# Optimization experiments

Measured on AMD Instinct MI355X. Metric: run time of the kernel, lower is better.

Reference implementation:

```python
import jax, jax.numpy as jnp
import numpy as np

EPS = 1e-5
N_HEADS = 8


def _ln(x, g, b):
    m = jnp.mean(x, -1, keepdims=True)
    v = jnp.mean((x - m) ** 2, -1, keepdims=True)
    return (x - m) * jax.lax.rsqrt(v + EPS) * g + b


def setup_inputs() -> dict:
    key = jax.random.key(0)
    ks = jax.random.split(key, 24)
    B, T, H = 64, 512, 256
    HH, H2 = H // 2, 2 * H
    w = lambda k, shape, fan_in: jax.random.normal(k, shape, jnp.float32) / np.sqrt(fan_in)
    return {
        "state": jax.random.normal(ks[0], (B, T, H), jnp.float32),
        "action": jax.random.normal(ks[1], (B, T, 2), jnp.float32),
        "ae_w1": w(ks[2], (2, HH), 2), "ae_b1": jnp.zeros((HH,), jnp.float32),
        "ae_w2": w(ks[3], (HH, H), HH), "ae_b2": jnp.zeros((H,), jnp.float32),
        "ln1_g": jnp.ones((H,), jnp.float32), "ln1_b": jnp.zeros((H,), jnp.float32),
        "ln2_g": jnp.ones((H,), jnp.float32), "ln2_b": jnp.zeros((H,), jnp.float32),
        "wq": w(ks[4], (H, H), H), "bq": jnp.zeros((H,), jnp.float32),
        "wk": w(ks[5], (H, H), H), "bk": jnp.zeros((H,), jnp.float32),
        "wv": w(ks[6], (H, H), H), "bv": jnp.zeros((H,), jnp.float32),
        "wo": w(ks[7], (H, H), H), "bo": jnp.zeros((H,), jnp.float32),
        "gru_wih": w(ks[8], (H, 3 * H2), H), "gru_bih": jnp.zeros((3 * H2,), jnp.float32),
        "gru_whh": w(ks[9], (H2, 3 * H2), H2), "gru_bhh": jnp.zeros((3 * H2,), jnp.float32),
        "mlp_w": w(ks[10], (H2, H), H2), "mlp_b": jnp.zeros((H,), jnp.float32),
    }


def reference(state, action, ae_w1, ae_b1, ae_w2, ae_b2, ln1_g, ln1_b, ln2_g, ln2_b,
              wq, bq, wk, bk, wv, bv, wo, bo,
              gru_wih, gru_bih, gru_whh, gru_bhh, mlp_w, mlp_b):
    B, T, H = state.shape
    dH = H // N_HEADS
    # action encoder (vectorized over all timesteps at once)
    ae = jax.nn.relu(action @ ae_w1 + ae_b1) @ ae_w2 + ae_b2  # [B,T,H]
    q_in = _ln(state, ln1_g, ln1_b)
    kv_in = _ln(ae, ln2_g, ln2_b)
    qh = (q_in @ wq + bq).reshape(B, T, N_HEADS, dH)
    kh = (kv_in @ wk + bk).reshape(B, T, N_HEADS, dH)
    vh = (kv_in @ wv + bv).reshape(B, T, N_HEADS, dH)
    # single query / single key per (b,t): softmax over the length-1 key axis == 1
    scores = jnp.sum(qh * kh, -1, keepdims=True) / jnp.sqrt(jnp.asarray(dH, state.dtype))
    attn = jax.nn.softmax(scores, axis=-1)  # [B,T,nH,1] of ones
    attended = (attn * vh).reshape(B, T, H) @ wo + bo
    x = state + attended  # [B,T,H]
    # GRU: original uses batch_first=False on a [B,T,H] tensor, so the
    # recurrence runs over dim 0 (B) with T as the effective batch.
    H2 = gru_whh.shape[0]

    def step(h, x_t):  # h,[T,2H]; x_t [T,H]
        gi = x_t @ gru_wih + gru_bih
        gh = h @ gru_whh + gru_bhh
        i_r, i_z, i_n = jnp.split(gi, 3, -1)
        h_r, h_z, h_n = jnp.split(gh, 3, -1)
        r = jax.nn.sigmoid(i_r + h_r)
        z = jax.nn.sigmoid(i_z + h_z)
        n = jnp.tanh(i_n + r * h_n)
        h_new = (1.0 - z) * n + z * h
        return h_new, h_new

    h0 = jnp.zeros((T, H2), x.dtype)
    _, out = jax.lax.scan(step, h0, x)  # [B,T,2H]
    states = out @ mlp_w + mlp_b  # dropout is identity in eval mode
    return states, states[:, -1]
```

## Files before the change

kernel.cpp:

```cpp
#include <hip/hip_runtime.h>
#include <hip/hip_bf16.h>

typedef unsigned short u16;
typedef unsigned long long u64;
typedef __attribute__((ext_vector_type(8))) short bf16x8;
typedef __attribute__((ext_vector_type(4))) float f32x4;

static __device__ __forceinline__ u16 f2bf(float f) {
    union { float f; unsigned u; } cv; cv.f = f;
    unsigned u = cv.u;
    unsigned r = u + 0x7FFF + ((u >> 16) & 1);
    return (u16)(r >> 16);
}
static __device__ __forceinline__ float bf2f(u16 b) {
    union { unsigned u; float f; } cv; cv.u = ((unsigned)b) << 16;
    return cv.f;
}
static __device__ __forceinline__ float sigmoidf_(float x) {
    return 1.0f / (1.0f + __expf(-x));
}
static __device__ __forceinline__ float tanhf_(float x) {
    float e = __expf(-2.f * fabsf(x));
    float t = (1.f - e) / (1.f + e);
    return copysignf(t, x);
}

__global__ __launch_bounds__(256) void prep_all(
    const float* __restrict__ wv, const float* __restrict__ wo,
    const float* __restrict__ wih, const float* __restrict__ whh,
    const float* __restrict__ mlp, const float* __restrict__ w2,
    const float* __restrict__ bv, const float* __restrict__ bo,
    u16* __restrict__ WfT, u16* __restrict__ wihT,
    u16* __restrict__ whhT, u16* __restrict__ mlpT, u16* __restrict__ w2T,
    float* __restrict__ bfv, u16* __restrict__ h0_bf,
    unsigned* __restrict__ flags)
{
    __shared__ u16 t[64][66];
    int bid = blockIdx.x, tid = threadIdx.x;

    if (bid >= 458) {
        int j = bid - 458, i = tid;
        float s = 0.f;
        for (int k = 0; k < 256; ++k) s = fmaf(wv[i * 256 + k], wo[k * 256 + j], s);
        WfT[j * 256 + i] = f2bf(s);
        return;
    }
    if (bid == 328) {
        int j = tid;
        float s = bo[j];
        for (int k = 0; k < 256; ++k) s = fmaf(bv[k], wo[k * 256 + j], s);
        bfv[j] = s;
        return;
    }
    if (bid >= 329 && bid < 457) {
        int i = ((bid - 329) * 256 + tid) * 2;
        u64* p = (u64*)h0_bf;
        p[i] = 0; p[i + 1] = 0;
        return;
    }
    if (bid == 457) {
        unsigned* p = flags;
        for (int i = tid; i < 32 * 8 * 32; i += 256) p[i] = 0u;
        return;
    }

    const float* src; u16* dst; int K, N, bx, by;
    if (bid < 96)       { src = wih; dst = wihT; K = 256; N = 1536; int l = bid;       bx = l & 3; by = l >> 2; }
    else if (bid < 288) { src = whh; dst = whhT; K = 512; N = 1536; int l = bid - 96;  bx = l & 7; by = l >> 3; }
    else if (bid < 320) { src = mlp; dst = mlpT; K = 512; N = 256;  int l = bid - 288; bx = l & 7; by = l >> 3; }
    else                { src = w2;  dst = w2T;  K = 128; N = 256;  int l = bid - 320; bx = l & 1; by = l >> 1; }

    int k0 = bx * 64, n0 = by * 64;
    int r = tid >> 4, c4 = (tid & 15) * 4;
#pragma unroll
    for (int p = 0; p < 4; ++p) {
        int row = r + p * 16;
        float4 v = *(const float4*)&src[(size_t)(k0 + row) * N + n0 + c4];
        t[c4 + 0][row] = f2bf(v.x);
        t[c4 + 1][row] = f2bf(v.y);
        t[c4 + 2][row] = f2bf(v.z);
        t[c4 + 3][row] = f2bf(v.w);
    }
    __syncthreads();
    int rr = tid >> 3, cc = (tid & 7) * 8;
#pragma unroll
    for (int p = 0; p < 2; ++p) {
        int row = rr + p * 32;
        u16 pack[8];
#pragma unroll
        for (int j = 0; j < 8; ++j) pack[j] = t[row][cc + j];
        *(uint4*)&dst[(size_t)(n0 + row) * K + k0 + cc] = *(uint4*)pack;
    }
}

__global__ __launch_bounds__(256) void ae_ln_mfma(
    const float* __restrict__ action,
    const float* __restrict__ w1, const float* __restrict__ b1,
    const u16* __restrict__ w2T, const float* __restrict__ b2,
    const float* __restrict__ g, const float* __restrict__ be,
    u16* __restrict__ kvbf)
{
    __shared__ u16 lB[256][136];
    __shared__ u16 lA[64][136];
    int tid = threadIdx.x;
    long base = (long)blockIdx.x * 64;

    for (int idx = tid; idx < 256 * 16; idx += 256) {
        int r = idx >> 4, ch = (idx & 15) * 8;
        *(uint4*)&lB[r][ch] = *(const uint4*)&w2T[r * 128 + ch];
    }
    for (int idx = tid; idx < 8192; idx += 256) {
        int r = idx >> 7, k = idx & 127;
        float a0 = action[(base + r) * 2], a1 = action[(base + r) * 2 + 1];
        float v = fmaf(a1, w1[128 + k], fmaf(a0, w1[k], b1[k]));
        lA[r][k] = f2bf(v > 0.f ? v : 0.f);
    }
    __syncthreads();

    int wv = tid >> 6, l = tid & 63;
    int fr = l & 15, fq = l >> 4;
    f32x4 acc[4][4] = {};
#pragma unroll
    for (int ks = 0; ks < 4; ++ks) {
        bf16x8 a[4], b[4];
#pragma unroll
        for (int mi = 0; mi < 4; ++mi) a[mi] = *(bf16x8*)&lA[mi * 16 + fr][ks * 32 + fq * 8];
#pragma unroll
        for (int ni = 0; ni < 4; ++ni) b[ni] = *(bf16x8*)&lB[wv * 64 + ni * 16 + fr][ks * 32 + fq * 8];
#pragma unroll
        for (int mi = 0; mi < 4; ++mi)
#pragma unroll
            for (int ni = 0; ni < 4; ++ni)
                acc[mi][ni] = __builtin_amdgcn_mfma_f32_16x16x32_bf16(a[mi], b[ni], acc[mi][ni], 0, 0, 0);
    }
    __syncthreads();

    float* e = (float*)&lB[0][0];
#pragma unroll
    for (int mi = 0; mi < 4; ++mi)
#pragma unroll
        for (int ni = 0; ni < 4; ++ni) {
            int col = wv * 64 + ni * 16 + fr;
            float bb = b2[col];
#pragma unroll
            for (int reg = 0; reg < 4; ++reg)
                e[(mi * 16 + fq * 4 + reg) * 261 + col] = acc[mi][ni][reg] + bb;
        }
    __syncthreads();

    int t = tid >> 2, sub = tid & 3;
    float s = 0.f, ss = 0.f;
#pragma unroll
    for (int i = 0; i < 64; ++i) {
        float v = e[t * 261 + sub + i * 4];
        s += v; ss += v * v;
    }
    s += __shfl_xor(s, 1); ss += __shfl_xor(ss, 1);
    s += __shfl_xor(s, 2); ss += __shfl_xor(ss, 2);
    float m = s * (1.f / 256.f);
    float var = ss * (1.f / 256.f) - m * m;
    float rs = rsqrtf(var + 1e-5f);
#pragma unroll
    for (int i8 = 0; i8 < 8; ++i8) {
        u16 pack[8];
#pragma unroll
        for (int j = 0; j < 8; ++j) {
            int col = sub * 64 + i8 * 8 + j;
            float v = (e[t * 261 + col] - m) * rs * g[col] + be[col];
            pack[j] = f2bf(v);
        }
        *(uint4*)&kvbf[(base + t) * 256 + sub * 64 + i8 * 8] = *(uint4*)pack;
    }
}

template <int MODE>
__global__ __launch_bounds__(256) void gemm128(
    const u16* __restrict__ A, const u16* __restrict__ BT,
    const float* __restrict__ bias, const float* __restrict__ resid,
    u16* __restrict__ outBf, float* __restrict__ outF,
    int N, int K)
{
    __shared__ u16 lA[128][72];
    __shared__ u16 lB[128][72];
    int tid = threadIdx.x;
    int bm = blockIdx.x * 128, bn = blockIdx.y * 128;

    f32x4 acc[4][4] = {};
    int w = tid >> 6, l = tid & 63;
    int wr = (w >> 1) * 64, wc = (w & 1) * 64;
    int fr = l & 15, fk = (l >> 4) * 8;

    for (int k0 = 0; k0 < K; k0 += 64) {
#pragma unroll
        for (int i = 0; i < 4; ++i) {
            int idx = tid + i * 256;
            int r = idx >> 3, c8 = (idx & 7) * 8;
            *(uint4*)&lA[r][c8] = *(const uint4*)&A[(long)(bm + r) * K + k0 + c8];
            *(uint4*)&lB[r][c8] = *(const uint4*)&BT[(long)(bn + r) * K + k0 + c8];
        }
        __syncthreads();
#pragma unroll
        for (int half = 0; half < 2; ++half) {
            int fo = half * 32 + fk;
            bf16x8 a[4], b[4];
#pragma unroll
            for (int mi = 0; mi < 4; ++mi) a[mi] = *(bf16x8*)&lA[wr + mi * 16 + fr][fo];
#pragma unroll
            for (int ni = 0; ni < 4; ++ni) b[ni] = *(bf16x8*)&lB[wc + ni * 16 + fr][fo];
#pragma unroll
            for (int mi = 0; mi < 4; ++mi)
#pragma unroll
                for (int ni = 0; ni < 4; ++ni)
                    acc[mi][ni] = __builtin_amdgcn_mfma_f32_16x16x32_bf16(a[mi], b[ni], acc[mi][ni], 0, 0, 0);
        }
        __syncthreads();
    }

#pragma unroll
    for (int mi = 0; mi < 4; ++mi)
#pragma unroll
        for (int ni = 0; ni < 4; ++ni) {
            int c = bn + wc + ni * 16 + fr;
            float bz = bias[c];
#pragma unroll
            for (int reg = 0; reg < 4; ++reg) {
                int r = bm + wr + mi * 16 + (l >> 4) * 4 + reg;
                float v = acc[mi][ni][reg] + bz;
                if constexpr (MODE == 0) {
                    v += resid[(long)r * N + c];
                    outBf[(long)r * N + c] = f2bf(v);
                } else if constexpr (MODE == 1) {
                    outBf[(long)r * N + c] = f2bf(v);
                } else {
                    outF[(long)r * N + c] = v;
                    if ((r & 511) == 511) outF[8388608 + (long)(r >> 9) * N + c] = v;
                }
            }
        }
}

__global__ __launch_bounds__(768, 1) void gru_persistent6(
    const u16* __restrict__ whhT, const float* __restrict__ bhh,
    const u16* __restrict__ gi_bf, const u16* __restrict__ h0_bf,
    u16* __restrict__ out_bf, unsigned* __restrict__ flags)
{
    __shared__ u64 lh64[2048];
    __shared__ __align__(16) float ghs[3][16][68];
    u16* lh = (u16*)lh64;

    int tid = threadIdx.x;
    int bid = blockIdx.x;
    int tg = bid >> 3, cb = bid & 7;
    int tbase = tg * 16, cbase = cb * 64;

    int w = tid >> 6, l = tid & 63;
    int fr = l & 15, fo = l >> 4;
    int cpos = w & 3, gate = w >> 2;

    bf16x8 a[16];
    {
        const u16* wp = whhT + ((size_t)(gate << 9) + cbase + cpos * 16 + fr) * 512 + fo * 8;
#pragma unroll
        for (int kk = 0; kk < 16; ++kk)
            a[kk] = *(const bf16x8*)(wp + kk * 32);
    }

    int et = tid >> 5, ec = (tid & 31) * 2;
    bool ep = tid < 512;
    float hreg0 = 0.f, hreg1 = 0.f;
    float bh_r0 = 0, bh_r1 = 0, bh_z0 = 0, bh_z1 = 0, bh_n0 = 0, bh_n1 = 0;
    if (ep) {
        bh_r0 = bhh[cbase + ec];        bh_r1 = bhh[cbase + ec + 1];
        bh_z0 = bhh[512 + cbase + ec];  bh_z1 = bhh[512 + cbase + ec + 1];
        bh_n0 = bhh[1024 + cbase + ec]; bh_n1 = bhh[1024 + cbase + ec + 1];
    }

    const unsigned* gp = (const unsigned*)gi_bf;
    unsigned g_r = 0, g_z = 0, g_n = 0;
    if (ep) {
        size_t grow = (size_t)(tbase + et) * 1536;
        g_r = gp[(grow + cbase + ec) >> 1];
        g_z = gp[(grow + 512 + cbase + ec) >> 1];
        g_n = gp[(grow + 1024 + cbase + ec) >> 1];
    }

    for (int step = 0; step < 64; ++step) {
        const u64* hb64 = (const u64*)(step ? out_bf + (size_t)(step - 1) * 262144
                                           : h0_bf);
#pragma unroll
        for (int i = 0; i < 3; ++i) {
            int idx = tid + i * 768;
            if (idx < 2048) {
                int r = idx >> 7, kw = idx & 127;
                u64 v = __hip_atomic_load(hb64 + (size_t)(tbase + r) * 128 + kw,
                                          __ATOMIC_RELAXED, __HIP_MEMORY_SCOPE_AGENT);
                lh64[r * 128 + (kw ^ ((r & 7) << 1))] = v;
            }
        }
        __syncthreads();

        f32x4 acc = {0.f, 0.f, 0.f, 0.f};
#pragma unroll
        for (int kk = 0; kk < 16; ++kk) {
            int kb = kk * 32 + fo * 8;
            bf16x8 b = *(bf16x8*)&lh[fr * 512 + (kb ^ ((fr & 7) << 3))];
            acc = __builtin_amdgcn_mfma_f32_16x16x32_bf16(a[kk], b, acc, 0, 0, 0);
        }
        *(f32x4*)&ghs[gate][fr][cpos * 16 + fo * 4] = acc;
        __syncthreads();

        if (ep) {
            float ghr0 = ghs[0][et][ec], ghr1 = ghs[0][et][ec + 1];
            float ghz0 = ghs[1][et][ec], ghz1 = ghs[1][et][ec + 1];
            float ghn0 = ghs[2][et][ec], ghn1 = ghs[2][et][ec + 1];
            float r0 = sigmoidf_(bf2f((u16)(g_r & 0xffff)) + ghr0 + bh_r0);
            float r1 = sigmoidf_(bf2f((u16)(g_r >> 16)) + ghr1 + bh_r1);
            float z0 = sigmoidf_(bf2f((u16)(g_z & 0xffff)) + ghz0 + bh_z0);
            float z1 = sigmoidf_(bf2f((u16)(g_z >> 16)) + ghz1 + bh_z1);
            float n0 = tanhf_(bf2f((u16)(g_n & 0xffff)) + r0 * (ghn0 + bh_n0));
            float n1 = tanhf_(bf2f((u16)(g_n >> 16)) + r1 * (ghn1 + bh_n1));
            hreg0 = (1.f - z0) * n0 + z0 * hreg0;
            hreg1 = (1.f - z1) * n1 + z1 * hreg1;
            unsigned packv = (unsigned)f2bf(hreg0) | ((unsigned)f2bf(hreg1) << 16);
            __hip_atomic_store(
                (unsigned*)out_bf + ((((size_t)step * 512 + tbase + et) * 512 + cbase + ec) >> 1),
                packv, __ATOMIC_RELAXED, __HIP_MEMORY_SCOPE_AGENT);
        }
        __syncthreads();

        if (step < 63) {
            if (tid == 0)
                __hip_atomic_store(&flags[(tg * 8 + cb) * 32], (unsigned)(step + 1),
                                   __ATOMIC_RELAXED, __HIP_MEMORY_SCOPE_AGENT);
            if (ep) {
                size_t grow = ((size_t)(step + 1) * 512 + tbase + et) * 1536;
                g_r = gp[(grow + cbase + ec) >> 1];
                g_z = gp[(grow + 512 + cbase + ec) >> 1];
                g_n = gp[(grow + 1024 + cbase + ec) >> 1];
            }
            if (tid < 8) {
                unsigned tgt = (unsigned)(step + 1);
                while (__hip_atomic_load(&flags[(tg * 8 + tid) * 32],
                                         __ATOMIC_RELAXED, __HIP_MEMORY_SCOPE_AGENT) < tgt)
                    __builtin_amdgcn_s_sleep(1);
            }
            __syncthreads();
        }
    }
}

extern "C" void kernel_launch(void* const* d_in, const int* in_sizes, int n_in,
                              void* d_out, int out_size, void* d_ws, size_t ws_size,
                              hipStream_t stream)
{
    const float* state   = (const float*)d_in[0];
    const float* action  = (const float*)d_in[1];
    const float* ae_w1   = (const float*)d_in[2];
    const float* ae_b1   = (const float*)d_in[3];
    const float* ae_w2   = (const float*)d_in[4];
    const float* ae_b2   = (const float*)d_in[5];
    const float* ln2_g   = (const float*)d_in[8];
    const float* ln2_b   = (const float*)d_in[9];
    const float* wv      = (const float*)d_in[14];
    const float* bv      = (const float*)d_in[15];
    const float* wo      = (const float*)d_in[16];
    const float* bo      = (const float*)d_in[17];
    const float* gru_wih = (const float*)d_in[18];
    const float* gru_bih = (const float*)d_in[19];
    const float* gru_whh = (const float*)d_in[20];
    const float* gru_bhh = (const float*)d_in[21];
    const float* mlp_w   = (const float*)d_in[22];
    const float* mlp_b   = (const float*)d_in[23];

    char* ws = (char*)d_ws;
    size_t off = 0;
    auto carve = [&](size_t bytes) -> char* {
        char* p = ws + off; off = (off + bytes + 255) & ~(size_t)255; return p;
    };
    u16*   kv_bf  = (u16*)carve(32768ull * 256 * 2);
    u16*   x_bf   = (u16*)carve(32768ull * 256 * 2);
    u16*   gi_bf  = (u16*)carve(32768ull * 1536 * 2);
    u16*   out_bf = (u16*)carve(32768ull * 512 * 2);
    u16*   WfT    = (u16*)carve(256 * 256 * 2);
    float* bfv    = (float*)carve(256 * 4);
    u16*   wihT   = (u16*)carve(1536 * 256 * 2);
    u16*   whhT   = (u16*)carve(1536 * 512 * 2);
    u16*   mlpT   = (u16*)carve(256 * 512 * 2);
    u16*   w2T    = (u16*)carve(256 * 128 * 2);
    u16*   h0_bf  = (u16*)carve(512 * 512 * 2);
    unsigned* flags = (unsigned*)carve(32 * 8 * 32 * 4);

    prep_all<<<714, 256, 0, stream>>>(wv, wo, gru_wih, gru_whh, mlp_w, ae_w2,
                                      bv, bo, WfT, wihT, whhT, mlpT, w2T,
                                      bfv, h0_bf, flags);

    ae_ln_mfma<<<512, 256, 0, stream>>>(action, ae_w1, ae_b1, w2T, ae_b2,
                                        ln2_g, ln2_b, kv_bf);

    gemm128<0><<<dim3(256, 2), 256, 0, stream>>>(kv_bf, WfT, bfv, state, x_bf, nullptr, 256, 256);
    gemm128<1><<<dim3(256, 12), 256, 0, stream>>>(x_bf, wihT, gru_bih, nullptr, gi_bf, nullptr, 1536, 256);

    {
        void* args[] = { (void*)&whhT, (void*)&gru_bhh, (void*)&gi_bf,
                         (void*)&h0_bf, (void*)&out_bf, (void*)&flags };
        hipError_t cerr = hipLaunchCooperativeKernel((const void*)gru_persistent6,
                                                     dim3(256), dim3(768), args, 0, stream);
        if (cerr != hipSuccess) {
            gru_persistent6<<<dim3(256), dim3(768), 0, stream>>>(
                whhT, gru_bhh, gi_bf, h0_bf, out_bf, flags);
        }
    }

    gemm128<2><<<dim3(256, 2), 256, 0, stream>>>(out_bf, mlpT, mlp_b, nullptr, nullptr,
                                                 (float*)d_out, 256, 512);
}
```

Before: 358.4 us.

## Fuse GRU input projection into persistent recurrent kernel

Measured after the change: 606.4 us. 69.2% more time.

```diff
diff --git a/kernel.cpp b/kernel.cpp
--- a/kernel.cpp
+++ b/kernel.cpp
@@ -239,13 +239,15 @@
         }
 }
 
-__global__ __launch_bounds__(768, 1) void gru_persistent6(
-    const u16* __restrict__ whhT, const float* __restrict__ bhh,
-    const u16* __restrict__ gi_bf, const u16* __restrict__ h0_bf,
+__global__ __launch_bounds__(768, 1) void gru_persistent11(
+    const u16* __restrict__ whhT, const u16* __restrict__ wihT,
+    const float* __restrict__ bhh, const float* __restrict__ bih,
+    const u16* __restrict__ x_bf, const u16* __restrict__ h0_bf,
     u16* __restrict__ out_bf, unsigned* __restrict__ flags)
 {
     __shared__ u64 lh64[2048];
     __shared__ __align__(16) float ghs[3][16][68];
+    __shared__ __align__(16) float gis[3][16][68];
     u16* lh = (u16*)lh64;
 
     int tid = threadIdx.x;
@@ -264,25 +266,42 @@
         for (int kk = 0; kk < 16; ++kk)
             a[kk] = *(const bf16x8*)(wp + kk * 32);
     }
+    const u16* wp2 = wihT + ((size_t)(gate << 9) + cbase + cpos * 16 + fr) * 256 + fo * 8;
 
     int et = tid >> 5, ec = (tid & 31) * 2;
     bool ep = tid < 512;
     float hreg0 = 0.f, hreg1 = 0.f;
-    float bh_r0 = 0, bh_r1 = 0, bh_z0 = 0, bh_z1 = 0, bh_n0 = 0, bh_n1 = 0;
+    float bs_r0 = 0, bs_r1 = 0, bs_z0 = 0, bs_z1 = 0;
+    float bi_n0 = 0, bi_n1 = 0, bh_n0 = 0, bh_n1 = 0;
     if (ep) {
-        bh_r0 = bhh[cbase + ec];        bh_r1 = bhh[cbase + ec + 1];
-        bh_z0 = bhh[512 + cbase + ec];  bh_z1 = bhh[512 + cbase + ec + 1];
-        bh_n0 = bhh[1024 + cbase + ec]; bh_n1 = bhh[1024 + cbase + ec + 1];
-    }
-
-    const unsigned* gp = (const unsigned*)gi_bf;
-    unsigned g_r = 0, g_z = 0, g_n = 0;
-    if (ep) {
-        size_t grow = (size_t)(tbase + et) * 1536;
-        g_r = gp[(grow + cbase + ec) >> 1];
-        g_z = gp[(grow + 512 + cbase + ec) >> 1];
-        g_n = gp[(grow + 1024 + cbase + ec) >> 1];
-    }
+        bs_r0 = bih[cbase + ec] + bhh[cbase + ec];
+        bs_r1 = bih[cbase + ec + 1] + bhh[cbase + ec + 1];
+        bs_z0 = bih[512 + cbase + ec] + bhh[512 + cbase + ec];
+        bs_z1 = bih[512 + cbase + ec + 1] + bhh[512 + cbase + ec + 1];
+        bi_n0 = bih[1024 + cbase + ec];  bi_n1 = bih[1024 + cbase + ec + 1];
+        bh_n0 = bhh[1024 + cbase + ec];  bh_n1 = bhh[1024 + cbase + ec + 1];
+    }
+
+    auto gi_compute = [&](int t) {
+        const u16* xp = x_bf + ((size_t)t * 512 + tbase + fr) * 256 + fo * 8;
+        f32x4 gacc = {0.f, 0.f, 0.f, 0.f};
+#pragma unroll
+        for (int half = 0; half < 2; ++half) {
+            bf16x8 xf[4], wf[4];
+#pragma unroll
+            for (int j = 0; j < 4; ++j) {
+                int kk = half * 4 + j;
+                xf[j] = *(const bf16x8*)(xp + kk * 32);
+                wf[j] = *(const bf16x8*)(wp2 + kk * 32);
+            }
+#pragma unroll
+            for (int j = 0; j < 4; ++j)
+                gacc = __builtin_amdgcn_mfma_f32_16x16x32_bf16(wf[j], xf[j], gacc, 0, 0, 0);
+        }
+        *(f32x4*)&gis[gate][fr][cpos * 16 + fo * 4] = gacc;
+    };
+
+    gi_compute(0);
 
     for (int step = 0; step < 64; ++step) {
         const u64* hb64 = (const u64*)(step ? out_bf + (size_t)(step - 1) * 262144
@@ -310,15 +329,12 @@
         __syncthreads();
 
         if (ep) {
-            float ghr0 = ghs[0][et][ec], ghr1 = ghs[0][et][ec + 1];
-            float ghz0 = ghs[1][et][ec], ghz1 = ghs[1][et][ec + 1];
-            float ghn0 = ghs[2][et][ec], ghn1 = ghs[2][et][ec + 1];
-            float r0 = sigmoidf_(bf2f((u16)(g_r & 0xffff)) + ghr0 + bh_r0);
-            float r1 = sigmoidf_(bf2f((u16)(g_r >> 16)) + ghr1 + bh_r1);
-            float z0 = sigmoidf_(bf2f((u16)(g_z & 0xffff)) + ghz0 + bh_z0);
-            float z1 = sigmoidf_(bf2f((u16)(g_z >> 16)) + ghz1 + bh_z1);
-            float n0 = tanhf_(bf2f((u16)(g_n & 0xffff)) + r0 * (ghn0 + bh_n0));
-            float n1 = tanhf_(bf2f((u16)(g_n >> 16)) + r1 * (ghn1 + bh_n1));
+            float r0 = sigmoidf_(gis[0][et][ec]     + ghs[0][et][ec]     + bs_r0);
+            float r1 = sigmoidf_(gis[0][et][ec + 1] + ghs[0][et][ec + 1] + bs_r1);
+            float z0 = sigmoidf_(gis[1][et][ec]     + ghs[1][et][ec]     + bs_z0);
+            float z1 = sigmoidf_(gis[1][et][ec + 1] + ghs[1][et][ec + 1] + bs_z1);
+            float n0 = tanhf_(gis[2][et][ec]     + bi_n0 + r0 * (ghs[2][et][ec]     + bh_n0));
+            float n1 = tanhf_(gis[2][et][ec + 1] + bi_n1 + r1 * (ghs[2][et][ec + 1] + bh_n1));
             hreg0 = (1.f - z0) * n0 + z0 * hreg0;
             hreg1 = (1.f - z1) * n1 + z1 * hreg1;
             unsigned packv = (unsigned)f2bf(hreg0) | ((unsigned)f2bf(hreg1) << 16);
@@ -332,12 +348,7 @@
             if (tid == 0)
                 __hip_atomic_store(&flags[(tg * 8 + cb) * 32], (unsigned)(step + 1),
                                    __ATOMIC_RELAXED, __HIP_MEMORY_SCOPE_AGENT);
-            if (ep) {
-                size_t grow = ((size_t)(step + 1) * 512 + tbase + et) * 1536;
-                g_r = gp[(grow + cbase + ec) >> 1];
-                g_z = gp[(grow + 512 + cbase + ec) >> 1];
-                g_n = gp[(grow + 1024 + cbase + ec) >> 1];
-            }
+            gi_compute(step + 1);
             if (tid < 8) {
                 unsigned tgt = (unsigned)(step + 1);
                 while (__hip_atomic_load(&flags[(tg * 8 + tid) * 32],
@@ -379,7 +390,6 @@
     };
     u16*   kv_bf  = (u16*)carve(32768ull * 256 * 2);
     u16*   x_bf   = (u16*)carve(32768ull * 256 * 2);
-    u16*   gi_bf  = (u16*)carve(32768ull * 1536 * 2);
     u16*   out_bf = (u16*)carve(32768ull * 512 * 2);
     u16*   WfT    = (u16*)carve(256 * 256 * 2);
     float* bfv    = (float*)carve(256 * 4);
@@ -398,16 +408,15 @@
                                         ln2_g, ln2_b, kv_bf);
 
     gemm128<0><<<dim3(256, 2), 256, 0, stream>>>(kv_bf, WfT, bfv, state, x_bf, nullptr, 256, 256);
-    gemm128<1><<<dim3(256, 12), 256, 0, stream>>>(x_bf, wihT, gru_bih, nullptr, gi_bf, nullptr, 1536, 256);
 
     {
-        void* args[] = { (void*)&whhT, (void*)&gru_bhh, (void*)&gi_bf,
-                         (void*)&h0_bf, (void*)&out_bf, (void*)&flags };
-        hipError_t cerr = hipLaunchCooperativeKernel((const void*)gru_persistent6,
+        void* args[] = { (void*)&whhT, (void*)&wihT, (void*)&gru_bhh, (void*)&gru_bih,
+                         (void*)&x_bf, (void*)&h0_bf, (void*)&out_bf, (void*)&flags };
+        hipError_t cerr = hipLaunchCooperativeKernel((const void*)gru_persistent11,
                                                      dim3(256), dim3(768), args, 0, stream);
         if (cerr != hipSuccess) {
-            gru_persistent6<<<dim3(256), dim3(768), 0, stream>>>(
-                whhT, gru_bhh, gi_bf, h0_bf, out_bf, flags);
+            gru_persistent11<<<dim3(256), dim3(768), 0, stream>>>(
+                whhT, wihT, gru_bhh, gru_bih, x_bf, h0_bf, out_bf, flags);
         }
     }
 
```
